# Kernel tuning notes

Measured on AMD Instinct MI355X. Metric: run time of the kernel, lower is better.

## Reference

```python
import jax, jax.numpy as jnp
import numpy as np

N, D, IN, OUT, K = 50000, 16, 256, 128, 4  # nodes, sampled degree, input_size, output_size, heads
LEAKY_SLOPE = 0.01  # torch F.leaky_relu default


def setup_inputs() -> dict:
    key = jax.random.key(0)
    k1, k2, k3, k4 = jax.random.split(key, 4)
    X = jax.random.normal(k1, (N, IN), dtype=jnp.float32)
    W = jax.random.normal(k2, (K, OUT, IN), dtype=jnp.float32) * 0.05
    a = jax.random.normal(k3, (K, 2 * OUT), dtype=jnp.float32) * 0.05
    neighbor_idx = jax.random.randint(k4, (N, D), 0, N)  # fixed-degree neighbor sample
    return {"X": X, "W": W, "a": a, "neighbor_idx": neighbor_idx}


def reference(X, W, a, neighbor_idx):
    # X: [N, IN]; W: [K, OUT, IN]; a: [K, 2*OUT]; neighbor_idx: [N, D]
    out_dim = W.shape[1]
    # Per-head linear map of every node once: Wh[k, n] = W[k] @ X[n]
    Wh = jnp.einsum('koi,ni->kno', W, X)                       # [K, N, OUT]
    # a splits: first OUT weights multiply mapped neighbour, second OUT multiply mapped self
    a_nb, a_self = a[:, :out_dim], a[:, out_dim:]
    e_nb = jnp.einsum('kno,ko->kn', Wh, a_nb)                  # [K, N] score contribution as a neighbour
    e_self = jnp.einsum('kno,ko->kn', Wh, a_self)              # [K, N] score contribution as center node
    # Edge logits: e[k, i, d] = leaky_relu(a_nb.Wh[j] + a_self.Wh[i]), j = neighbor_idx[i, d]
    e = jax.nn.leaky_relu(e_nb[:, neighbor_idx] + e_self[:, :, None], LEAKY_SLOPE)  # [K, N, D]
    alpha = jax.nn.softmax(e, axis=-1)                         # softmax over each node's neighbour set
    Wh_nb = jnp.take(Wh, neighbor_idx, axis=1)                 # [K, N, D, OUT] gathered neighbour features
    h = jnp.einsum('knd,kndo->kno', alpha, Wh_nb)              # [K, N, OUT] attention-weighted aggregate
    # Concatenate heads along feature dim, matching per-node head-concat in the torch loop
    return jnp.transpose(h, (1, 0, 2)).reshape(X.shape[0], -1)  # [N, K*OUT]
```

## Files before the change

### kernel.cpp

```cpp
#include <hip/hip_runtime.h>

#define N_NODES 50000
#define D_NB 16
#define IN_DIM 256
#define OUT_DIM 128
#define K_HEADS 4
#define SLOPE 0.01f
#define NSLICE 16
#define SLICE_COLS 32

typedef __attribute__((ext_vector_type(8))) short short8;
typedef __attribute__((ext_vector_type(4))) float f32x4;

static __device__ __forceinline__ unsigned short f2bf(float f) {
    unsigned u = __float_as_uint(f);
    unsigned r = u + 0x7fffu + ((u >> 16) & 1u);
    return (unsigned short)(r >> 16);
}
static __device__ __forceinline__ float bf2f(unsigned short b) {
    return __uint_as_float(((unsigned)b) << 16);
}

__global__ void wb_kernel(const float* __restrict__ W, unsigned short* __restrict__ Wb) {
    int id = blockIdx.x * blockDim.x + threadIdx.x;
    if (id < K_HEADS * OUT_DIM * IN_DIM) Wb[id] = f2bf(W[id]);
}

__global__ __launch_bounds__(256) void gemm_kernel(
    const float* __restrict__ X, const unsigned short* __restrict__ Wb,
    const float* __restrict__ a,
    unsigned short* __restrict__ Whb2, float* __restrict__ e_nb, float* __restrict__ e_self)
{
    __shared__ unsigned short Wlds[2][SLICE_COLS * IN_DIM];

    const int t = threadIdx.x;
    const int lane = t & 63;
    const int w = t >> 6;
    const int lrow = lane & 15;
    const int lk = lane >> 4;
    const int m0 = blockIdx.x * 64 + w * 16;

    const int arow = m0 + lrow;
    const bool avalid = arow < N_NODES;

    const float* Xr = X + (size_t)arow * IN_DIM + lk * 8;
    short8 af[8];
    #pragma unroll
    for (int kk = 0; kk < 8; ++kk) {
        short8 s;
        if (avalid) {
            float4 x0 = *(const float4*)(Xr + kk * 32);
            float4 x1 = *(const float4*)(Xr + kk * 32 + 4);
            s[0] = (short)f2bf(x0.x); s[1] = (short)f2bf(x0.y);
            s[2] = (short)f2bf(x0.z); s[3] = (short)f2bf(x0.w);
            s[4] = (short)f2bf(x1.x); s[5] = (short)f2bf(x1.y);
            s[6] = (short)f2bf(x1.z); s[7] = (short)f2bf(x1.w);
        } else {
            s = short8{0, 0, 0, 0, 0, 0, 0, 0};
        }
        af[kk] = s;
    }

    auto STAGE = [&](int st, int buf) {
        const unsigned short* WbS = Wb + (size_t)st * SLICE_COLS * IN_DIM;
        #pragma unroll
        for (int i = 0; i < 4; ++i) {
            const int c = i * 256 + t;
            const int r = c >> 5;
            const int p = c & 31;
            const int cu = p ^ (r & 7);
            const unsigned short* gsrc = WbS + r * IN_DIM + cu * 8;
            unsigned short* ldst = &Wlds[buf][c * 8];
            __builtin_amdgcn_global_load_lds(
                (const __attribute__((address_space(1))) void*)gsrc,
                (__attribute__((address_space(3))) void*)ldst, 16, 0, 0);
        }
    };

    float pnb = 0.f, psf = 0.f;
    STAGE(0, 0);
    __syncthreads();

    for (int st = 0; st < NSLICE; ++st) {
        const int buf = st & 1;
        if (st + 1 < NSLICE) STAGE(st + 1, buf ^ 1);

        f32x4 acc[2] = {};
        #pragma unroll
        for (int kk = 0; kk < 8; ++kk) {
            #pragma unroll
            for (int nt = 0; nt < 2; ++nt) {
                const int row = nt * 16 + lrow;
                const int pos = (kk * 4 + lk) ^ (row & 7);
                const short8 bf = *(const short8*)(&Wlds[buf][row * IN_DIM + pos * 8]);
                acc[nt] = __builtin_amdgcn_mfma_f32_16x16x32_bf16(bf, af[kk], acc[nt], 0, 0, 0);
            }
        }

        const int k = st >> 2, cb = st & 3;
        #pragma unroll
        for (int nt = 0; nt < 2; ++nt) {
            const float4 anb = *(const float4*)(a + k * 2 * OUT_DIM + cb * 32 + nt * 16 + lk * 4);
            const float4 asf = *(const float4*)(a + k * 2 * OUT_DIM + OUT_DIM + cb * 32 + nt * 16 + lk * 4);
            pnb += acc[nt][0] * anb.x + acc[nt][1] * anb.y
                 + acc[nt][2] * anb.z + acc[nt][3] * anb.w;
            psf += acc[nt][0] * asf.x + acc[nt][1] * asf.y
                 + acc[nt][2] * asf.z + acc[nt][3] * asf.w;
            if (avalid) {
                uint2 pk;
                pk.x = (unsigned)f2bf(acc[nt][0]) | ((unsigned)f2bf(acc[nt][1]) << 16);
                pk.y = (unsigned)f2bf(acc[nt][2]) | ((unsigned)f2bf(acc[nt][3]) << 16);
                *(uint2*)(Whb2 + ((size_t)st * N_NODES + arow) * SLICE_COLS + nt * 16 + lk * 4) = pk;
            }
        }
        if ((st & 3) == 3) {
            pnb += __shfl_xor(pnb, 16); pnb += __shfl_xor(pnb, 32);
            psf += __shfl_xor(psf, 16); psf += __shfl_xor(psf, 32);
            if (avalid && lane < 16) {
                e_nb[(size_t)arow * K_HEADS + k] = pnb;
                e_self[(size_t)arow * K_HEADS + k] = psf;
            }
            pnb = 0.f; psf = 0.f;
        }
        __syncthreads();
    }
}

__global__ __launch_bounds__(256) void attn_kernel(
    const int* __restrict__ nidx, const unsigned short* __restrict__ Whb2,
    const float* __restrict__ e_nb, const float* __restrict__ e_self,
    float* __restrict__ out)
{
    const int xcd = blockIdx.x & 7;
    const int slot = blockIdx.x >> 3;
    const int w = threadIdx.x >> 6;
    const int lane = threadIdx.x & 63;
    const int nl = lane >> 4;
    const int d = lane & 15;
    const int s0 = xcd * 2;
    const int k = s0 >> 2;
    const int cb0 = s0 & 3;
    const unsigned short* S0 = Whb2 + (size_t)s0 * N_NODES * SLICE_COLS;
    const unsigned short* S1 = S0 + (size_t)N_NODES * SLICE_COLS;

    for (int i = slot; i < N_NODES / 16; i += 128) {
        const int n = i * 16 + w * 4 + nl;

        const int nbr = nidx[(size_t)n * D_NB + d];
        const float x = e_nb[(size_t)nbr * K_HEADS + k] + e_self[(size_t)n * K_HEADS + k];
        const float v = x > 0.f ? x : SLOPE * x;
        float m = v;
        #pragma unroll
        for (int s = 8; s >= 1; s >>= 1) m = fmaxf(m, __shfl_xor(m, s, 16));
        const float p = __expf(v - m);
        float sum = p;
        #pragma unroll
        for (int s = 8; s >= 1; s >>= 1) sum += __shfl_xor(sum, s, 16);
        const float alpha = p / sum;

        float a0 = 0.f, a1 = 0.f, a2 = 0.f, a3 = 0.f;
        #pragma unroll
        for (int dd = 0; dd < D_NB; ++dd) {
            const int src = (lane & 48) | dd;
            const float ad = __shfl(alpha, src);
            const int nd = __shfl(nbr, src);
            const unsigned u0 = *(const unsigned*)(S0 + (size_t)nd * SLICE_COLS + d * 2);
            const unsigned u1 = *(const unsigned*)(S1 + (size_t)nd * SLICE_COLS + d * 2);
            a0 += ad * bf2f((unsigned short)(u0 & 0xffffu));
            a1 += ad * bf2f((unsigned short)(u0 >> 16));
            a2 += ad * bf2f((unsigned short)(u1 & 0xffffu));
            a3 += ad * bf2f((unsigned short)(u1 >> 16));
        }
        float* op = out + (size_t)n * (K_HEADS * OUT_DIM) + k * OUT_DIM + cb0 * SLICE_COLS + d * 2;
        *(float2*)op        = float2{a0, a1};
        *(float2*)(op + 32) = float2{a2, a3};
    }
}

extern "C" void kernel_launch(void* const* d_in, const int* in_sizes, int n_in,
                              void* d_out, int out_size, void* d_ws, size_t ws_size,
                              hipStream_t stream) {
    const float* X = (const float*)d_in[0];
    const float* W = (const float*)d_in[1];
    const float* a = (const float*)d_in[2];
    const int* nidx = (const int*)d_in[3];
    float* out = (float*)d_out;

    char* p = (char*)d_ws;
    unsigned short* Wb = (unsigned short*)p;      p += (size_t)K_HEADS * OUT_DIM * IN_DIM * 2;
    unsigned short* Whb2 = (unsigned short*)p;    p += (size_t)NSLICE * N_NODES * SLICE_COLS * 2;
    float* enb = (float*)p;                       p += (size_t)N_NODES * K_HEADS * 4;
    float* eself = (float*)p;

    hipLaunchKernelGGL(wb_kernel,
        dim3((K_HEADS * OUT_DIM * IN_DIM + 255) / 256), dim3(256), 0, stream, W, Wb);

    hipLaunchKernelGGL(gemm_kernel,
        dim3((N_NODES + 63) / 64), dim3(256), 0, stream, X, Wb, a, Whb2, enb, eself);

    hipLaunchKernelGGL(attn_kernel,
        dim3(8 * 128), dim3(256), 0, stream, nidx, Whb2, enb, eself, out);
}
```

Measured before the change: 192.5 us.

## Process one slice per XCD pass and double attention grid slots

```diff
diff --git a/kernel.cpp b/kernel.cpp
--- a/kernel.cpp
+++ b/kernel.cpp
@@ -8,9 +8,11 @@
 #define SLOPE 0.01f
 #define NSLICE 16
 #define SLICE_COLS 32
+#define NSLOT 256
 
 typedef __attribute__((ext_vector_type(8))) short short8;
 typedef __attribute__((ext_vector_type(4))) float f32x4;
+typedef __attribute__((ext_vector_type(2))) float f32x2;
 
 static __device__ __forceinline__ unsigned short f2bf(float f) {
     unsigned u = __float_as_uint(f);
@@ -137,43 +139,45 @@
     const int lane = threadIdx.x & 63;
     const int nl = lane >> 4;
     const int d = lane & 15;
-    const int s0 = xcd * 2;
-    const int k = s0 >> 2;
-    const int cb0 = s0 & 3;
-    const unsigned short* S0 = Whb2 + (size_t)s0 * N_NODES * SLICE_COLS;
-    const unsigned short* S1 = S0 + (size_t)N_NODES * SLICE_COLS;
-
-    for (int i = slot; i < N_NODES / 16; i += 128) {
-        const int n = i * 16 + w * 4 + nl;
-
-        const int nbr = nidx[(size_t)n * D_NB + d];
-        const float x = e_nb[(size_t)nbr * K_HEADS + k] + e_self[(size_t)n * K_HEADS + k];
-        const float v = x > 0.f ? x : SLOPE * x;
-        float m = v;
-        #pragma unroll
-        for (int s = 8; s >= 1; s >>= 1) m = fmaxf(m, __shfl_xor(m, s, 16));
-        const float p = __expf(v - m);
-        float sum = p;
-        #pragma unroll
-        for (int s = 8; s >= 1; s >>= 1) sum += __shfl_xor(sum, s, 16);
-        const float alpha = p / sum;
-
-        float a0 = 0.f, a1 = 0.f, a2 = 0.f, a3 = 0.f;
-        #pragma unroll
-        for (int dd = 0; dd < D_NB; ++dd) {
-            const int src = (lane & 48) | dd;
-            const float ad = __shfl(alpha, src);
-            const int nd = __shfl(nbr, src);
-            const unsigned u0 = *(const unsigned*)(S0 + (size_t)nd * SLICE_COLS + d * 2);
-            const unsigned u1 = *(const unsigned*)(S1 + (size_t)nd * SLICE_COLS + d * 2);
-            a0 += ad * bf2f((unsigned short)(u0 & 0xffffu));
-            a1 += ad * bf2f((unsigned short)(u0 >> 16));
-            a2 += ad * bf2f((unsigned short)(u1 & 0xffffu));
-            a3 += ad * bf2f((unsigned short)(u1 >> 16));
-        }
-        float* op = out + (size_t)n * (K_HEADS * OUT_DIM) + k * OUT_DIM + cb0 * SLICE_COLS + d * 2;
-        *(float2*)op        = float2{a0, a1};
-        *(float2*)(op + 32) = float2{a2, a3};
+
+    #pragma unroll
+    for (int p = 0; p < 2; ++p) {
+        const int s = xcd + p * 8;
+        const int k = s >> 2;
+        const int cb = s & 3;
+        const unsigned short* S = Whb2 + (size_t)s * N_NODES * SLICE_COLS;
+
+        for (int i = slot; i < N_NODES / 16; i += NSLOT) {
+            const int n = i * 16 + w * 4 + nl;
+
+            const int nbr = __builtin_nontemporal_load(nidx + (size_t)n * D_NB + d);
+            const float es = __builtin_nontemporal_load(e_self + (size_t)n * K_HEADS + k);
+            const float x = e_nb[(size_t)nbr * K_HEADS + k] + es;
+            const float v = x > 0.f ? x : SLOPE * x;
+            float m = v;
+            #pragma unroll
+            for (int sh = 8; sh >= 1; sh >>= 1) m = fmaxf(m, __shfl_xor(m, sh, 16));
+            const float pz = __expf(v - m);
+            float sum = pz;
+            #pragma unroll
+            for (int sh = 8; sh >= 1; sh >>= 1) sum += __shfl_xor(sum, sh, 16);
+            const float alpha = pz / sum;
+
+            float a0 = 0.f, a1 = 0.f;
+            #pragma unroll
+            for (int dd = 0; dd < D_NB; ++dd) {
+                const int src = (lane & 48) | dd;
+                const float ad = __shfl(alpha, src);
+                const int nd = __shfl(nbr, src);
+                const unsigned u = *(const unsigned*)(S + (size_t)nd * SLICE_COLS + d * 2);
+                a0 += ad * bf2f((unsigned short)(u & 0xffffu));
+                a1 += ad * bf2f((unsigned short)(u >> 16));
+            }
+            f32x2* op = (f32x2*)(out + (size_t)n * (K_HEADS * OUT_DIM) + k * OUT_DIM
+                                 + cb * SLICE_COLS + d * 2);
+            __builtin_nontemporal_store(f32x2{a0, a1}, op);
+        }
+        __syncthreads();
     }
 }
 
@@ -199,5 +203,5 @@
         dim3((N_NODES + 63) / 64), dim3(256), 0, stream, X, Wb, a, Whb2, enb, eself);
 
     hipLaunchKernelGGL(attn_kernel,
-        dim3(8 * 128), dim3(256), 0, stream, nidx, Whb2, enb, eself, out);
-}
+        dim3(8 * NSLOT), dim3(256), 0, stream, nidx, Whb2, enb, eself, out);
+}
```

Result: slower. 231.5 us (+20.3%).
